# Performance work log

Hardware: AMD Instinct MI355X
Metric: run time of the kernel (lower is better)

Reference implementation:

```python
import jax, jax.numpy as jnp
import numpy as np

EPS_STAB = 1e-9   # numerical_stabilizer default
BN_EPS = 1e-5     # flax BatchNorm default epsilon


def setup_inputs() -> dict:
    key = jax.random.key(0)
    ks = jax.random.split(key, 5)
    B, N, C = 2, 4096, 512
    s = 1.0 / np.sqrt(C)
    d = {"inputs": jax.random.normal(ks[0], (B, N, C), jnp.float32)}
    # 1x1 convs == pointwise linear maps [C_in, C_out] + bias
    for i, w in enumerate(["Wq", "Wk", "Wv", "Wo"]):
        d[w] = jax.random.normal(ks[1 + i], (C, C), jnp.float32) * s
    for b in ["bq", "bk", "bv", "bo"]:
        d[b] = jnp.zeros((C,), jnp.float32)
    # BatchNorm (inference: use_running_average=True since train=False)
    d["bn_scale"] = jnp.ones((C,), jnp.float32)
    d["bn_bias"] = jnp.zeros((C,), jnp.float32)
    d["bn_mean"] = jnp.zeros((C,), jnp.float32)
    d["bn_var"] = jnp.ones((C,), jnp.float32)
    return d


def reference(inputs, Wq, bq, Wk, bk, Wv, bv, Wo, bo,
              bn_scale, bn_bias, bn_mean, bn_var):
    # QKV via 1x1 conv == dense projection. [B, N, C]
    q = inputs @ Wq + bq
    k = inputs @ Wk + bk
    v = inputs @ Wv + bv
    # scores [B, M, N]; softmax over last axis (N)
    att = jax.nn.softmax(jnp.einsum('bmc,bnc->bmn', q, k), axis=-1)
    # non-standard renorm: divide by column sums (axis=1 == M axis)
    att = att / (EPS_STAB + jnp.sum(att, axis=1, keepdims=True))
    # faithful to einsum '...MN,...NC->...NC': sum attention over M, scale v
    out = v * jnp.sum(att, axis=1)[..., None]
    # output 1x1 conv
    out = out @ Wo + bo
    # BatchNorm with running stats (feature axis -1)
    out = (out - bn_mean) * jax.lax.rsqrt(bn_var + BN_EPS) * bn_scale + bn_bias
    return jax.nn.relu(out) + inputs
```

## Files before the change

kernel.cpp:

```cpp
#include <hip/hip_runtime.h>
#include <hip/hip_bf16.h>

typedef unsigned short u16;
typedef unsigned int u32;
typedef __attribute__((ext_vector_type(8))) short short8;
typedef __attribute__((ext_vector_type(4))) float f32x4;
typedef __attribute__((ext_vector_type(4))) unsigned int u32x4;

__device__ __forceinline__ u16 f2bf(float f) {
    union { float f; unsigned u; } v; v.f = f;
    unsigned r = v.u + 0x7fffu + ((v.u >> 16) & 1u);
    return (u16)(r >> 16);
}

__device__ __forceinline__ float fexp2(float x) {
#if __has_builtin(__builtin_amdgcn_exp2f)
    return __builtin_amdgcn_exp2f(x);
#else
    return __expf(x * 0.6931471805599453f);
#endif
}

template <int CTRL>
__device__ __forceinline__ float fdpp(float x) {
    int xi = __builtin_bit_cast(int, x);
    int r = __builtin_amdgcn_update_dpp(0, xi, CTRL, 0xF, 0xF, true);
    return __builtin_bit_cast(float, r);
}
__device__ __forceinline__ float dpp_max16(float m) {
    m = fmaxf(m, fdpp<0xB1>(m));
    m = fmaxf(m, fdpp<0x4E>(m));
    m = fmaxf(m, fdpp<0x141>(m));
    m = fmaxf(m, fdpp<0x140>(m));
    return m;
}
__device__ __forceinline__ float dpp_sum16(float s) {
    s += fdpp<0xB1>(s);
    s += fdpp<0x4E>(s);
    s += fdpp<0x141>(s);
    s += fdpp<0x140>(s);
    return s;
}

#if __has_builtin(__builtin_amdgcn_cvt_pk_fp8_f32) && \
    __has_builtin(__builtin_amdgcn_cvt_f32_fp8)
#define FP8_HW 1
#else
#define FP8_HW 0
#endif

#if !FP8_HW
__device__ __forceinline__ u32 sw_fp8(float x) {
    union { float f; u32 u; } v; v.f = x;
    int E = (int)(v.u >> 23) - 127;
    if (x < 0.001953125f) return 0;
    if (E < -6) return (u32)(x * 512.0f + 0.5f);
    u32 m = v.u & 0x7fffffu;
    u32 r = (m + 0x80000u) >> 20;
    u32 bits = ((u32)(E + 7) << 3) + r;
    return bits > 0x7eu ? 0x7eu : bits;
}
__device__ __forceinline__ float sw_fp8d(u32 b) {
    u32 e = (b >> 3) & 15u, m = b & 7u;
    if (e == 0) return (float)m * 0.001953125f;
    union { u32 u; float f; } v; v.u = ((e + 120u) << 23) | (m << 20);
    return v.f;
}
#endif

__device__ __forceinline__ u32 fp8x4_pack(float p0, float p1, float p2, float p3) {
#if FP8_HW
    u32 v = (u32)__builtin_amdgcn_cvt_pk_fp8_f32(p0, p1, 0, false);
    v = (u32)__builtin_amdgcn_cvt_pk_fp8_f32(p2, p3, (int)v, true);
    return v;
#else
    return sw_fp8(p0) | (sw_fp8(p1) << 8) | (sw_fp8(p2) << 16) | (sw_fp8(p3) << 24);
#endif
}

#if FP8_HW
#define FP8_DEC(v, s) __builtin_amdgcn_cvt_f32_fp8((int)(v), (s))
#else
#define FP8_DEC(v, s) sw_fp8d(((v) >> ((s) * 8)) & 0xffu)
#endif

__device__ __forceinline__ void async_cp16(const u16* g, u16* l) {
    __builtin_amdgcn_global_load_lds(
        (const __attribute__((address_space(1))) void*)g,
        (__attribute__((address_space(3))) void*)l, 16, 0, 0);
}

__device__ __forceinline__ short8 mfma_ld(const u16* base, int off) {
    return *(const short8*)&base[off];
}

__device__ __forceinline__ void gemm512(const u16* __restrict__ A,
                                        const u16* __restrict__ B,
                                        u16* As, u16* Bs,
                                        f32x4 acc[4][4], int tid) {
    const int lane = tid & 63, w = tid >> 6;
    const int quad = lane >> 4, l15 = lane & 15;
    const int wm = tid >> 7, wn = (tid >> 6) & 1;
    const int Gw = lane ^ ((lane >> 3) & 7);
    const int srow = Gw >> 3;
    const int scol = (Gw & 7) * 8;
    const int rl = l15 & 7;
    const int winl = l15 >> 3;
    int Pr[2];
#pragma unroll
    for (int h = 0; h < 2; h++)
        Pr[h] = (rl * 8 + ((quad + h * 4) ^ rl)) * 8;
    const int winA0 = (wm * 64) >> 3, winB0 = (wn * 64) >> 3;
    for (int k0 = 0; k0 < 512; k0 += 64) {
        __syncthreads();
#pragma unroll
        for (int t = 0; t < 4; t++) {
            int win = w * 4 + t;
            async_cp16(A + (size_t)(win * 8 + srow) * 512 + k0 + scol,
                       As + win * 512);
            async_cp16(B + (size_t)(win * 8 + srow) * 512 + k0 + scol,
                       Bs + win * 512);
        }
        __syncthreads();
#pragma unroll
        for (int h = 0; h < 2; h++) {
            short8 af[4], bfr[4];
#pragma unroll
            for (int i = 0; i < 4; i++)
                af[i] = mfma_ld(As, (winA0 + i * 2 + winl) * 512 + Pr[h]);
#pragma unroll
            for (int j = 0; j < 4; j++)
                bfr[j] = mfma_ld(Bs, (winB0 + j * 2 + winl) * 512 + Pr[h]);
#pragma unroll
            for (int i = 0; i < 4; i++)
#pragma unroll
                for (int j = 0; j < 4; j++)
                    acc[i][j] = __builtin_amdgcn_mfma_f32_16x16x32_bf16(
                        af[i], bfr[j], acc[i][j], 0, 0, 0);
        }
    }
}

__device__ __forceinline__ void gemm512_r64(const u16* __restrict__ A,
                                            const u16* __restrict__ B,
                                            u16* As, u16* Bs,
                                            f32x4 acc[2][4], int tid) {
    const int lane = tid & 63, w = tid >> 6;
    const int quad = lane >> 4, l15 = lane & 15;
    const int wm = tid >> 7, wn = (tid >> 6) & 1;
    const int Gw = lane ^ ((lane >> 3) & 7);
    const int srow = Gw >> 3;
    const int scol = (Gw & 7) * 8;
    const int rl = l15 & 7;
    const int winl = l15 >> 3;
    int Pr[2];
#pragma unroll
    for (int h = 0; h < 2; h++)
        Pr[h] = (rl * 8 + ((quad + h * 4) ^ rl)) * 8;
    const int winA0 = (wm * 32) >> 3, winB0 = (wn * 64) >> 3;
    for (int k0 = 0; k0 < 512; k0 += 64) {
        __syncthreads();
#pragma unroll
        for (int t = 0; t < 2; t++) {
            int win = w * 2 + t;
            async_cp16(A + (size_t)(win * 8 + srow) * 512 + k0 + scol,
                       As + win * 512);
        }
#pragma unroll
        for (int t = 0; t < 4; t++) {
            int win = w * 4 + t;
            async_cp16(B + (size_t)(win * 8 + srow) * 512 + k0 + scol,
                       Bs + win * 512);
        }
        __syncthreads();
#pragma unroll
        for (int h = 0; h < 2; h++) {
            short8 af[2], bfr[4];
#pragma unroll
            for (int i = 0; i < 2; i++)
                af[i] = mfma_ld(As, (winA0 + i * 2 + winl) * 512 + Pr[h]);
#pragma unroll
            for (int j = 0; j < 4; j++)
                bfr[j] = mfma_ld(Bs, (winB0 + j * 2 + winl) * 512 + Pr[h]);
#pragma unroll
            for (int i = 0; i < 2; i++)
#pragma unroll
                for (int j = 0; j < 4; j++)
                    acc[i][j] = __builtin_amdgcn_mfma_f32_16x16x32_bf16(
                        af[i], bfr[j], acc[i][j], 0, 0, 0);
        }
    }
}

__global__ void prep(const float* __restrict__ X, const float* __restrict__ W0,
                     const float* __restrict__ W1, const float* __restrict__ W2,
                     const float* __restrict__ W3, u16* __restrict__ Xb,
                     u16* __restrict__ T0, u16* __restrict__ T1,
                     u16* __restrict__ T2, u16* __restrict__ T3,
                     float* __restrict__ Sg) {
    __shared__ float tile[32][33];
    int id = blockIdx.x, tid = threadIdx.x;
    if (id == 5120) {
        float4 z = {0.f, 0.f, 0.f, 0.f};
#pragma unroll
        for (int t = 0; t < 8; t++) ((float4*)Sg)[tid + t * 256] = z;
        return;
    }
    if (id < 4096) {
        int idx = (id * 256 + tid) * 4;
        float4 v = *(const float4*)&X[idx];
        ushort4 o;
        o.x = f2bf(v.x); o.y = f2bf(v.y); o.z = f2bf(v.z); o.w = f2bf(v.w);
        *(ushort4*)&Xb[idx] = o;
        return;
    }
    int t = id - 4096;
    int z = t >> 8, rem = t & 255;
    int bo_ = (rem & 15) * 32, bi = (rem >> 4) * 32;
    const float* src; u16* dst;
    switch (z) {
        case 0: src = W0; dst = T0; break;
        case 1: src = W1; dst = T1; break;
        case 2: src = W2; dst = T2; break;
        default: src = W3; dst = T3; break;
    }
    int tx = tid & 31, ty = tid >> 5;
#pragma unroll
    for (int s = 0; s < 4; s++) {
        int i = bi + ty + s * 8;
        tile[ty + s * 8][tx] = src[i * 512 + bo_ + tx];
    }
    __syncthreads();
#pragma unroll
    for (int s = 0; s < 4; s++) {
        int o = bo_ + ty + s * 8;
        dst[o * 512 + bi + tx] = f2bf(tile[tx][ty + s * 8]);
    }
}

__global__ __launch_bounds__(256) void gemm_qkv(
    const u16* __restrict__ Xb, const u16* __restrict__ Wall,
    const float* __restrict__ bq, const float* __restrict__ bk,
    const float* __restrict__ bv, u16* __restrict__ Qall) {
    __shared__ __align__(16) u16 As[8192];
    __shared__ __align__(16) u16 Bs[8192];
    int tid = threadIdx.x;
    int m0 = blockIdx.x * 128, n0 = blockIdx.y * 128, z = blockIdx.z;
    const u16* Bt = Wall + (size_t)z * 262144 + (size_t)n0 * 512;
    const float* bias = (z == 0) ? bq : (z == 1) ? bk : bv;
    const float qs = (z == 0) ? 1.44269504088896340736f : 1.0f;
    u16* C = Qall + (size_t)z * 4194304;
    f32x4 acc[4][4];
#pragma unroll
    for (int i = 0; i < 4; i++)
#pragma unroll
        for (int j = 0; j < 4; j++) acc[i][j] = (f32x4){0.f, 0.f, 0.f, 0.f};
    gemm512(Xb + (size_t)m0 * 512, Bt, As, Bs, acc, tid);
    int lane = tid & 63, quad = lane >> 4, l15 = lane & 15;
    int wm = tid >> 7, wn = (tid >> 6) & 1;
#pragma unroll
    for (int j = 0; j < 4; j++) {
        int n = n0 + wn * 64 + j * 16 + l15;
        float bvv = bias[n];
#pragma unroll
        for (int i = 0; i < 4; i++)
#pragma unroll
            for (int rg = 0; rg < 4; rg++) {
                int m = m0 + wm * 64 + i * 16 + quad * 4 + rg;
                C[(size_t)m * 512 + n] = f2bf((acc[i][j][rg] + bvv) * qs);
            }
    }
}

__device__ __forceinline__ void stage_half_A(const u16* __restrict__ Q,
                                             u16* dst, int kn, int half,
                                             int wid, int srow, int scol) {
#pragma unroll
    for (int c = 0; c < 2; c++) {
        int win = (wid >> 2) * 16 + half * 8 + (wid & 3) * 2 + c;
        async_cp16(Q + (size_t)(win * 8 + srow) * 512 + kn + scol,
                   dst + win * 512);
    }
}
__device__ __forceinline__ void stage_half_B(const u16* __restrict__ K,
                                             u16* dst, int kn, int half,
                                             int wid, int srow, int scol) {
#pragma unroll
    for (int c = 0; c < 2; c++) {
        int win = (wid >> 1) * 8 + half * 4 + (wid & 1) * 2 + c;
        async_cp16(K + (size_t)(win * 8 + srow) * 512 + kn + scol,
                   dst + win * 512);
    }
}

__global__ __launch_bounds__(512, 2) void attn_pass1p(
    const u16* __restrict__ Qb, const u16* __restrict__ Kb,
    float2* __restrict__ statsP, u32* __restrict__ Pbuf) {
    __shared__ __align__(16) u16 As[2][16384];
    __shared__ __align__(16) u16 Bs[2][16384];
    int tid = threadIdx.x;
    int mblk = blockIdx.x, nblk = blockIdx.y, b = blockIdx.z;
    const u16* Q = Qb + ((size_t)(b * 4096 + mblk * 256)) * 512;
    const u16* K = Kb + ((size_t)(b * 4096 + nblk * 256)) * 512;
    int lane = tid & 63, wid = tid >> 6;
    int quad = lane >> 4, l15 = lane & 15;
    int wm = wid >> 2, wn = wid & 3;
    int Gw = lane ^ ((lane >> 3) & 7);
    int srow = Gw >> 3, scol = (Gw & 7) * 8;
    int rl = l15 & 7, winl = l15 >> 3;
    int Pr[2];
#pragma unroll
    for (int h = 0; h < 2; h++)
        Pr[h] = (rl * 8 + ((quad + h * 4) ^ rl)) * 8;

    f32x4 acc[8][4];
#pragma unroll
    for (int i = 0; i < 8; i++)
#pragma unroll
        for (int j = 0; j < 4; j++) acc[i][j] = (f32x4){0.f, 0.f, 0.f, 0.f};

    stage_half_A(Q, &As[0][0], 0, 0, wid, srow, scol);
    stage_half_B(K, &Bs[0][0], 0, 0, wid, srow, scol);
    stage_half_B(K, &Bs[0][0], 0, 1, wid, srow, scol);
    stage_half_A(Q, &As[0][0], 0, 1, wid, srow, scol);
    asm volatile("s_waitcnt vmcnt(0)" ::: "memory");
    __builtin_amdgcn_s_barrier();
    asm volatile("" ::: "memory");

    for (int kt = 0; kt < 8; ++kt) {
        const u16* Ac = &As[kt & 1][0];
        const u16* Bc = &Bs[kt & 1][0];
        u16* An = &As[(kt + 1) & 1][0];
        u16* Bn = &Bs[(kt + 1) & 1][0];
        int kn = (kt + 1) * 64;
        bool pf = (kt < 7);
        short8 af[4][2], bf0[2][2], bf1[2][2];
#pragma unroll
        for (int ph = 0; ph < 4; ++ph) {
            const int ih = ph >> 1;
            const int jh = (ph ^ (ph >> 1)) & 1;
            if (ph == 0) {
#pragma unroll
                for (int h = 0; h < 2; h++)
#pragma unroll
                    for (int ii = 0; ii < 4; ii++)
                        af[ii][h] = mfma_ld(
                            Ac, (wm * 16 + ii * 2 + winl) * 512 + Pr[h]);
#pragma unroll
                for (int h = 0; h < 2; h++)
#pragma unroll
                    for (int jj = 0; jj < 2; jj++)
                        bf0[jj][h] = mfma_ld(
                            Bc, (wn * 8 + jj * 2 + winl) * 512 + Pr[h]);
            } else if (ph == 1) {
#pragma unroll
                for (int h = 0; h < 2; h++)
#pragma unroll
                    for (int jj = 0; jj < 2; jj++)
                        bf1[jj][h] = mfma_ld(
                            Bc, (wn * 8 + 4 + jj * 2 + winl) * 512 + Pr[h]);
            } else if (ph == 2) {
#pragma unroll
                for (int h = 0; h < 2; h++)
#pragma unroll
                    for (int ii = 0; ii < 4; ii++)
                        af[ii][h] = mfma_ld(
                            Ac, (wm * 16 + 8 + ii * 2 + winl) * 512 + Pr[h]);
            }
            if (pf) {
                if (ph == 0) {
                    stage_half_A(Q, An, kn, 0, wid, srow, scol);
                    stage_half_B(K, Bn, kn, 0, wid, srow, scol);
                } else if (ph == 1) {
                    stage_half_B(K, Bn, kn, 1, wid, srow, scol);
                } else if (ph == 2) {
                    stage_half_A(Q, An, kn, 1, wid, srow, scol);
                }
            }
            if (ph == 1) {
                if (pf) asm volatile("s_waitcnt vmcnt(6)" ::: "memory");
                else    asm volatile("s_waitcnt vmcnt(0)" ::: "memory");
            }
            if (ph == 3) asm volatile("s_waitcnt vmcnt(2)" ::: "memory");
            asm volatile("" ::: "memory");
            __builtin_amdgcn_s_barrier();
            asm volatile("s_waitcnt lgkmcnt(0)" ::: "memory");
            __builtin_amdgcn_s_setprio(1);
            if (jh == 0) {
#pragma unroll
                for (int h = 0; h < 2; h++)
#pragma unroll
                    for (int ii = 0; ii < 4; ii++)
#pragma unroll
                        for (int jj = 0; jj < 2; jj++)
                            acc[ih * 4 + ii][jj] =
                                __builtin_amdgcn_mfma_f32_16x16x32_bf16(
                                    af[ii][h], bf0[jj][h],
                                    acc[ih * 4 + ii][jj], 0, 0, 0);
            } else {
#pragma unroll
                for (int h = 0; h < 2; h++)
#pragma unroll
                    for (int ii = 0; ii < 4; ii++)
#pragma unroll
                        for (int jj = 0; jj < 2; jj++)
                            acc[ih * 4 + ii][2 + jj] =
                                __builtin_amdgcn_mfma_f32_16x16x32_bf16(
                                    af[ii][h], bf1[jj][h],
                                    acc[ih * 4 + ii][2 + jj], 0, 0, 0);
            }
            __builtin_amdgcn_s_setprio(0);
            asm volatile("" ::: "memory");
            __builtin_amdgcn_s_barrier();
            asm volatile("" ::: "memory");
        }
    }

    u32* Pt = Pbuf + ((size_t)((b * 16 + mblk) * 16 + nblk)) * 16384;
    int ch = nblk * 4 + wn;
    float2* Sp = statsP + ((size_t)(b * 64 + ch)) * 4096;
    int mbase = mblk * 256 + wm * 128;
#pragma unroll
    for (int i = 0; i < 8; i++) {
        u32x4 pk;
#pragma unroll
        for (int rg = 0; rg < 4; rg++) {
            float v0 = acc[i][0][rg], v1 = acc[i][1][rg];
            float v2 = acc[i][2][rg], v3 = acc[i][3][rg];
            float Mt = fmaxf(fmaxf(v0, v1), fmaxf(v2, v3));
            Mt = dpp_max16(Mt);
            float e8 = Mt - 8.0f;
            float p0 = fexp2(v0 - e8), p1 = fexp2(v1 - e8);
            float p2 = fexp2(v2 - e8), p3 = fexp2(v3 - e8);
            pk[rg] = fp8x4_pack(p0, p1, p2, p3);
            float L = dpp_sum16(p0 + p1 + p2 + p3);
            if (l15 == 0)
                Sp[mbase + i * 16 + quad * 4 + rg] =
                    make_float2(Mt, L * 0.00390625f);
        }
        *(u32x4*)&Pt[i * 2048 + tid * 4] = pk;
    }
}

__global__ void reduce_stats2(const float2* __restrict__ statsP,
                              float* __restrict__ cstat) {
    int t = blockIdx.x * 256 + threadIdx.x;
    int b = t >> 12, m = t & 4095;
    const float2* sp = statsP + (size_t)b * 64 * 4096 + m;
    float M = -INFINITY;
#pragma unroll 4
    for (int ch = 0; ch < 64; ch++) M = fmaxf(M, sp[(size_t)ch * 4096].x);
    float Z = 0.f;
#pragma unroll 4
    for (int ch = 0; ch < 64; ch++) {
        float2 p = sp[(size_t)ch * 4096];
        Z += p.y * fexp2(p.x - M);
    }
    cstat[t] = M + __log2f(Z);
}

__global__ __launch_bounds__(512) void colsum(
    const u32* __restrict__ Pbuf, const float2* __restrict__ statsP,
    const float* __restrict__ cstat, float* __restrict__ Sg) {
    int tid = threadIdx.x, lane = tid & 63, wid = tid >> 6;
    int quad = lane >> 4, l15 = lane & 15;
    int wm = wid >> 2, wn = wid & 3;
    int nblk = blockIdx.x, mgrp = blockIdx.y, b = blockIdx.z;
    int ch = nblk * 4 + wn;
    const float2* Sp = statsP + ((size_t)(b * 64 + ch)) * 4096;
    const float* Cp = cstat + (size_t)b * 4096;
    float cp[4] = {0.f, 0.f, 0.f, 0.f};
    for (int mb = 0; mb < 2; mb++) {
        int mblk = mgrp * 2 + mb;
        const u32* Pt =
            Pbuf + ((size_t)((b * 16 + mblk) * 16 + nblk)) * 16384;
#pragma unroll
        for (int i = 0; i < 8; i++) {
            int r0 = mblk * 256 + wm * 128 + i * 16 + quad * 4;
            float4 s01 = *(const float4*)&Sp[r0];
            float4 s23 = *(const float4*)&Sp[r0 + 2];
            float4 cv = *(const float4*)&Cp[r0];
            float fv[4] = {fexp2(s01.x - 8.0f - cv.x),
                           fexp2(s01.z - 8.0f - cv.y),
                           fexp2(s23.x - 8.0f - cv.z),
                           fexp2(s23.z - 8.0f - cv.w)};
            float fm = fmaxf(fmaxf(fv[0], fv[1]), fmaxf(fv[2], fv[3]));
            if (fm > 3.469446951953614e-18f) {
                u32x4 e4 = *(const u32x4*)&Pt[i * 2048 + tid * 4];
#pragma unroll
                for (int rg = 0; rg < 4; rg++) {
                    u32 e = e4[rg];
                    cp[0] += FP8_DEC(e, 0) * fv[rg];
                    cp[1] += FP8_DEC(e, 1) * fv[rg];
                    cp[2] += FP8_DEC(e, 2) * fv[rg];
                    cp[3] += FP8_DEC(e, 3) * fv[rg];
                }
            }
        }
    }
#pragma unroll
    for (int j = 0; j < 4; j++) {
        float s = cp[j];
        s += __shfl_xor(s, 16);
        s += __shfl_xor(s, 32);
        if (lane < 16)
            atomicAdd(&Sg[b * 4096 + nblk * 256 + wn * 64 + j * 16 + l15], s);
    }
}

__global__ __launch_bounds__(256) void gemm_final(
    const u16* __restrict__ A, const u16* __restrict__ Bt,
    const float* __restrict__ Sg, const float* __restrict__ bo,
    const float* __restrict__ g, const float* __restrict__ bb,
    const float* __restrict__ mean, const float* __restrict__ var,
    const float* __restrict__ X, float* __restrict__ out) {
    __shared__ __align__(16) u16 As[4096];
    __shared__ __align__(16) u16 Bs[8192];
    int tid = threadIdx.x;
    int m0 = blockIdx.x * 64, n0 = blockIdx.y * 128;
    f32x4 acc[2][4];
#pragma unroll
    for (int i = 0; i < 2; i++)
#pragma unroll
        for (int j = 0; j < 4; j++) acc[i][j] = (f32x4){0.f, 0.f, 0.f, 0.f};
    gemm512_r64(A + (size_t)m0 * 512, Bt + (size_t)n0 * 512, As, Bs, acc, tid);
    int lane = tid & 63, quad = lane >> 4, l15 = lane & 15;
    int wm = tid >> 7, wn = (tid >> 6) & 1;
    float sc[2][4];
#pragma unroll
    for (int i = 0; i < 2; i++) {
        float4 s = *(const float4*)&Sg[m0 + wm * 32 + i * 16 + quad * 4];
        float v[4] = {s.x, s.y, s.z, s.w};
#pragma unroll
        for (int rg = 0; rg < 4; rg++) sc[i][rg] = v[rg] / (1e-9f + v[rg]);
    }
#pragma unroll
    for (int j = 0; j < 4; j++) {
        int n = n0 + wn * 64 + j * 16 + l15;
        float aj = rsqrtf(var[n] + 1e-5f) * g[n];
        float cj = bb[n] - mean[n] * aj;
        float bj = bo[n];
#pragma unroll
        for (int i = 0; i < 2; i++)
#pragma unroll
            for (int rg = 0; rg < 4; rg++) {
                int m = m0 + wm * 32 + i * 16 + quad * 4 + rg;
                float x = acc[i][j][rg] * sc[i][rg] + bj;
                float y = x * aj + cj;
                out[(size_t)m * 512 + n] = fmaxf(y, 0.f) + X[(size_t)m * 512 + n];
            }
    }
}

extern "C" void kernel_launch(void* const* d_in, const int* in_sizes, int n_in,
                              void* d_out, int out_size, void* d_ws, size_t ws_size,
                              hipStream_t stream) {
    const float* X  = (const float*)d_in[0];
    const float* Wq = (const float*)d_in[1];
    const float* Wk = (const float*)d_in[2];
    const float* Wv = (const float*)d_in[3];
    const float* Wo = (const float*)d_in[4];
    const float* bq = (const float*)d_in[5];
    const float* bk = (const float*)d_in[6];
    const float* bv = (const float*)d_in[7];
    const float* bo = (const float*)d_in[8];
    const float* g    = (const float*)d_in[9];
    const float* bb   = (const float*)d_in[10];
    const float* mean = (const float*)d_in[11];
    const float* var  = (const float*)d_in[12];
    float* out = (float*)d_out;

    char* ws = (char*)d_ws;
    u16* Xb  = (u16*)(ws + 0);
    u16* Wqt = (u16*)(ws + 8388608);
    u16* Wot = (u16*)(ws + 9961472);
    u16* Qb  = (u16*)(ws + 10485760);
    u16* Kb  = (u16*)(ws + 18874368);
    u16* Vb  = (u16*)(ws + 27262976);
    float2* statsP = (float2*)(ws + 35651584);
    float* Sg      = (float*)(ws + 39845888);
    float* cstat   = (float*)(ws + 39878656);
    u32* Pbuf      = (u32*)(ws + 39911424);

    prep<<<5121, 256, 0, stream>>>(X, Wq, Wk, Wv, Wo, Xb, Wqt, Wqt + 262144,
                                   Wqt + 524288, Wot, Sg);
    gemm_qkv<<<dim3(64, 4, 3), 256, 0, stream>>>(Xb, Wqt, bq, bk, bv, Qb);
    attn_pass1p<<<dim3(16, 16, 2), 512, 0, stream>>>(Qb, Kb, statsP, Pbuf);
    reduce_stats2<<<32, 256, 0, stream>>>(statsP, cstat);
    colsum<<<dim3(16, 8, 2), 512, 0, stream>>>(Pbuf, statsP, cstat, Sg);
    gemm_final<<<dim3(128, 4), 256, 0, stream>>>(Vb, Wot, Sg, bo, g, bb, mean, var,
                                                 X, out);
}
```

Baseline: 203.9 us.

## Reuse pipelined 256x256 attention GEMM core for QKV projection

```diff
diff --git a/kernel.cpp b/kernel.cpp
--- a/kernel.cpp
+++ b/kernel.cpp
@@ -94,49 +94,137 @@
     return *(const short8*)&base[off];
 }
 
-__device__ __forceinline__ void gemm512(const u16* __restrict__ A,
+__device__ __forceinline__ void stage_half_A(const u16* __restrict__ Q,
+                                             u16* dst, int kn, int half,
+                                             int wid, int srow, int scol) {
+#pragma unroll
+    for (int c = 0; c < 2; c++) {
+        int win = (wid >> 2) * 16 + half * 8 + (wid & 3) * 2 + c;
+        async_cp16(Q + (size_t)(win * 8 + srow) * 512 + kn + scol,
+                   dst + win * 512);
+    }
+}
+__device__ __forceinline__ void stage_half_B(const u16* __restrict__ K,
+                                             u16* dst, int kn, int half,
+                                             int wid, int srow, int scol) {
+#pragma unroll
+    for (int c = 0; c < 2; c++) {
+        int win = (wid >> 1) * 8 + half * 4 + (wid & 1) * 2 + c;
+        async_cp16(K + (size_t)(win * 8 + srow) * 512 + kn + scol,
+                   dst + win * 512);
+    }
+}
+
+__device__ __forceinline__ void core256(const u16* __restrict__ A,
                                         const u16* __restrict__ B,
-                                        u16* As, u16* Bs,
-                                        f32x4 acc[4][4], int tid) {
-    const int lane = tid & 63, w = tid >> 6;
-    const int quad = lane >> 4, l15 = lane & 15;
-    const int wm = tid >> 7, wn = (tid >> 6) & 1;
-    const int Gw = lane ^ ((lane >> 3) & 7);
-    const int srow = Gw >> 3;
-    const int scol = (Gw & 7) * 8;
-    const int rl = l15 & 7;
-    const int winl = l15 >> 3;
+                                        u16* As0, u16* As1,
+                                        u16* Bs0, u16* Bs1,
+                                        f32x4 acc[8][4], int tid) {
+    int lane = tid & 63, wid = tid >> 6;
+    int quad = lane >> 4, l15 = lane & 15;
+    int wm = wid >> 2, wn = wid & 3;
+    int Gw = lane ^ ((lane >> 3) & 7);
+    int srow = Gw >> 3, scol = (Gw & 7) * 8;
+    int rl = l15 & 7, winl = l15 >> 3;
     int Pr[2];
 #pragma unroll
     for (int h = 0; h < 2; h++)
         Pr[h] = (rl * 8 + ((quad + h * 4) ^ rl)) * 8;
-    const int winA0 = (wm * 64) >> 3, winB0 = (wn * 64) >> 3;
-    for (int k0 = 0; k0 < 512; k0 += 64) {
-        __syncthreads();
-#pragma unroll
-        for (int t = 0; t < 4; t++) {
-            int win = w * 4 + t;
-            async_cp16(A + (size_t)(win * 8 + srow) * 512 + k0 + scol,
-                       As + win * 512);
-            async_cp16(B + (size_t)(win * 8 + srow) * 512 + k0 + scol,
-                       Bs + win * 512);
-        }
-        __syncthreads();
-#pragma unroll
-        for (int h = 0; h < 2; h++) {
-            short8 af[4], bfr[4];
-#pragma unroll
-            for (int i = 0; i < 4; i++)
-                af[i] = mfma_ld(As, (winA0 + i * 2 + winl) * 512 + Pr[h]);
-#pragma unroll
-            for (int j = 0; j < 4; j++)
-                bfr[j] = mfma_ld(Bs, (winB0 + j * 2 + winl) * 512 + Pr[h]);
-#pragma unroll
-            for (int i = 0; i < 4; i++)
-#pragma unroll
-                for (int j = 0; j < 4; j++)
-                    acc[i][j] = __builtin_amdgcn_mfma_f32_16x16x32_bf16(
-                        af[i], bfr[j], acc[i][j], 0, 0, 0);
+
+    stage_half_A(A, As0, 0, 0, wid, srow, scol);
+    stage_half_B(B, Bs0, 0, 0, wid, srow, scol);
+    stage_half_B(B, Bs0, 0, 1, wid, srow, scol);
+    stage_half_A(A, As0, 0, 1, wid, srow, scol);
+    asm volatile("s_waitcnt vmcnt(0)" ::: "memory");
+    __builtin_amdgcn_s_barrier();
+    asm volatile("" ::: "memory");
+
+    for (int kt = 0; kt < 8; ++kt) {
+        const u16* Ac = (kt & 1) ? As1 : As0;
+        const u16* Bc = (kt & 1) ? Bs1 : Bs0;
+        u16* An = (kt & 1) ? As0 : As1;
+        u16* Bn = (kt & 1) ? Bs0 : Bs1;
+        int kn = (kt + 1) * 64;
+        bool pf = (kt < 7);
+        short8 af[4][2], bf0[2][2], bf1[2][2];
+#pragma unroll
+        for (int ph = 0; ph < 4; ++ph) {
+            const int ih = ph >> 1;
+            const int jh = (ph ^ (ph >> 1)) & 1;
+            if (ph == 0) {
+#pragma unroll
+                for (int h = 0; h < 2; h++)
+#pragma unroll
+                    for (int ii = 0; ii < 4; ii++)
+                        af[ii][h] = mfma_ld(
+                            Ac, (wm * 16 + ii * 2 + winl) * 512 + Pr[h]);
+#pragma unroll
+                for (int h = 0; h < 2; h++)
+#pragma unroll
+                    for (int jj = 0; jj < 2; jj++)
+                        bf0[jj][h] = mfma_ld(
+                            Bc, (wn * 8 + jj * 2 + winl) * 512 + Pr[h]);
+            } else if (ph == 1) {
+#pragma unroll
+                for (int h = 0; h < 2; h++)
+#pragma unroll
+                    for (int jj = 0; jj < 2; jj++)
+                        bf1[jj][h] = mfma_ld(
+                            Bc, (wn * 8 + 4 + jj * 2 + winl) * 512 + Pr[h]);
+            } else if (ph == 2) {
+#pragma unroll
+                for (int h = 0; h < 2; h++)
+#pragma unroll
+                    for (int ii = 0; ii < 4; ii++)
+                        af[ii][h] = mfma_ld(
+                            Ac, (wm * 16 + 8 + ii * 2 + winl) * 512 + Pr[h]);
+            }
+            if (pf) {
+                if (ph == 0) {
+                    stage_half_A(A, An, kn, 0, wid, srow, scol);
+                    stage_half_B(B, Bn, kn, 0, wid, srow, scol);
+                } else if (ph == 1) {
+                    stage_half_B(B, Bn, kn, 1, wid, srow, scol);
+                } else if (ph == 2) {
+                    stage_half_A(A, An, kn, 1, wid, srow, scol);
+                }
+            }
+            if (ph == 1) {
+                if (pf) asm volatile("s_waitcnt vmcnt(6)" ::: "memory");
+                else    asm volatile("s_waitcnt vmcnt(0)" ::: "memory");
+            }
+            if (ph == 3) asm volatile("s_waitcnt vmcnt(2)" ::: "memory");
+            asm volatile("" ::: "memory");
+            __builtin_amdgcn_s_barrier();
+            asm volatile("s_waitcnt lgkmcnt(0)" ::: "memory");
+            __builtin_amdgcn_s_setprio(1);
+            if (jh == 0) {
+#pragma unroll
+                for (int h = 0; h < 2; h++)
+#pragma unroll
+                    for (int ii = 0; ii < 4; ii++)
+#pragma unroll
+                        for (int jj = 0; jj < 2; jj++)
+                            acc[ih * 4 + ii][jj] =
+                                __builtin_amdgcn_mfma_f32_16x16x32_bf16(
+                                    af[ii][h], bf0[jj][h],
+                                    acc[ih * 4 + ii][jj], 0, 0, 0);
+            } else {
+#pragma unroll
+                for (int h = 0; h < 2; h++)
+#pragma unroll
+                    for (int ii = 0; ii < 4; ii++)
+#pragma unroll
+                        for (int jj = 0; jj < 2; jj++)
+                            acc[ih * 4 + ii][2 + jj] =
+                                __builtin_amdgcn_mfma_f32_16x16x32_bf16(
+                                    af[ii][h], bf1[jj][h],
+                                    acc[ih * 4 + ii][2 + jj], 0, 0, 0);
+            }
+            __builtin_amdgcn_s_setprio(0);
+            asm volatile("" ::: "memory");
+            __builtin_amdgcn_s_barrier();
+            asm volatile("" ::: "memory");
         }
     }
 }
@@ -238,58 +326,40 @@
     }
 }
 
-__global__ __launch_bounds__(256) void gemm_qkv(
+__global__ __launch_bounds__(512, 2) void gemm_qkv(
     const u16* __restrict__ Xb, const u16* __restrict__ Wall,
     const float* __restrict__ bq, const float* __restrict__ bk,
     const float* __restrict__ bv, u16* __restrict__ Qall) {
-    __shared__ __align__(16) u16 As[8192];
-    __shared__ __align__(16) u16 Bs[8192];
+    __shared__ __align__(16) u16 As[2][16384];
+    __shared__ __align__(16) u16 Bs[2][16384];
     int tid = threadIdx.x;
-    int m0 = blockIdx.x * 128, n0 = blockIdx.y * 128, z = blockIdx.z;
-    const u16* Bt = Wall + (size_t)z * 262144 + (size_t)n0 * 512;
+    int m0 = blockIdx.x * 256, n0 = blockIdx.y * 256, z = blockIdx.z;
+    const u16* A = Xb + (size_t)m0 * 512;
+    const u16* B = Wall + (size_t)z * 262144 + (size_t)n0 * 512;
+    f32x4 acc[8][4];
+#pragma unroll
+    for (int i = 0; i < 8; i++)
+#pragma unroll
+        for (int j = 0; j < 4; j++) acc[i][j] = (f32x4){0.f, 0.f, 0.f, 0.f};
+    core256(A, B, &As[0][0], &As[1][0], &Bs[0][0], &Bs[1][0], acc, tid);
+
     const float* bias = (z == 0) ? bq : (z == 1) ? bk : bv;
     const float qs = (z == 0) ? 1.44269504088896340736f : 1.0f;
     u16* C = Qall + (size_t)z * 4194304;
-    f32x4 acc[4][4];
-#pragma unroll
-    for (int i = 0; i < 4; i++)
-#pragma unroll
-        for (int j = 0; j < 4; j++) acc[i][j] = (f32x4){0.f, 0.f, 0.f, 0.f};
-    gemm512(Xb + (size_t)m0 * 512, Bt, As, Bs, acc, tid);
-    int lane = tid & 63, quad = lane >> 4, l15 = lane & 15;
-    int wm = tid >> 7, wn = (tid >> 6) & 1;
+    int lane = tid & 63, wid = tid >> 6;
+    int quad = lane >> 4, l15 = lane & 15;
+    int wm = wid >> 2, wn = wid & 3;
 #pragma unroll
     for (int j = 0; j < 4; j++) {
         int n = n0 + wn * 64 + j * 16 + l15;
         float bvv = bias[n];
 #pragma unroll
-        for (int i = 0; i < 4; i++)
+        for (int i = 0; i < 8; i++)
 #pragma unroll
             for (int rg = 0; rg < 4; rg++) {
-                int m = m0 + wm * 64 + i * 16 + quad * 4 + rg;
+                int m = m0 + wm * 128 + i * 16 + quad * 4 + rg;
                 C[(size_t)m * 512 + n] = f2bf((acc[i][j][rg] + bvv) * qs);
             }
-    }
-}
-
-__device__ __forceinline__ void stage_half_A(const u16* __restrict__ Q,
-                                             u16* dst, int kn, int half,
-                                             int wid, int srow, int scol) {
-#pragma unroll
-    for (int c = 0; c < 2; c++) {
-        int win = (wid >> 2) * 16 + half * 8 + (wid & 3) * 2 + c;
-        async_cp16(Q + (size_t)(win * 8 + srow) * 512 + kn + scol,
-                   dst + win * 512);
-    }
-}
-__device__ __forceinline__ void stage_half_B(const u16* __restrict__ K,
-                                             u16* dst, int kn, int half,
-                                             int wid, int srow, int scol) {
-#pragma unroll
-    for (int c = 0; c < 2; c++) {
-        int win = (wid >> 1) * 8 + half * 4 + (wid & 1) * 2 + c;
-        async_cp16(K + (size_t)(win * 8 + srow) * 512 + kn + scol,
-                   dst + win * 512);
     }
 }
 
@@ -305,116 +375,13 @@
     int lane = tid & 63, wid = tid >> 6;
     int quad = lane >> 4, l15 = lane & 15;
     int wm = wid >> 2, wn = wid & 3;
-    int Gw = lane ^ ((lane >> 3) & 7);
-    int srow = Gw >> 3, scol = (Gw & 7) * 8;
-    int rl = l15 & 7, winl = l15 >> 3;
-    int Pr[2];
-#pragma unroll
-    for (int h = 0; h < 2; h++)
-        Pr[h] = (rl * 8 + ((quad + h * 4) ^ rl)) * 8;
 
     f32x4 acc[8][4];
 #pragma unroll
     for (int i = 0; i < 8; i++)
 #pragma unroll
         for (int j = 0; j < 4; j++) acc[i][j] = (f32x4){0.f, 0.f, 0.f, 0.f};
-
-    stage_half_A(Q, &As[0][0], 0, 0, wid, srow, scol);
-    stage_half_B(K, &Bs[0][0], 0, 0, wid, srow, scol);
-    stage_half_B(K, &Bs[0][0], 0, 1, wid, srow, scol);
-    stage_half_A(Q, &As[0][0], 0, 1, wid, srow, scol);
-    asm volatile("s_waitcnt vmcnt(0)" ::: "memory");
-    __builtin_amdgcn_s_barrier();
-    asm volatile("" ::: "memory");
-
-    for (int kt = 0; kt < 8; ++kt) {
-        const u16* Ac = &As[kt & 1][0];
-        const u16* Bc = &Bs[kt & 1][0];
-        u16* An = &As[(kt + 1) & 1][0];
-        u16* Bn = &Bs[(kt + 1) & 1][0];
-        int kn = (kt + 1) * 64;
-        bool pf = (kt < 7);
-        short8 af[4][2], bf0[2][2], bf1[2][2];
-#pragma unroll
-        for (int ph = 0; ph < 4; ++ph) {
-            const int ih = ph >> 1;
-            const int jh = (ph ^ (ph >> 1)) & 1;
-            if (ph == 0) {
-#pragma unroll
-                for (int h = 0; h < 2; h++)
-#pragma unroll
-                    for (int ii = 0; ii < 4; ii++)
-                        af[ii][h] = mfma_ld(
-                            Ac, (wm * 16 + ii * 2 + winl) * 512 + Pr[h]);
-#pragma unroll
-                for (int h = 0; h < 2; h++)
-#pragma unroll
-                    for (int jj = 0; jj < 2; jj++)
-                        bf0[jj][h] = mfma_ld(
-                            Bc, (wn * 8 + jj * 2 + winl) * 512 + Pr[h]);
-            } else if (ph == 1) {
-#pragma unroll
-                for (int h = 0; h < 2; h++)
-#pragma unroll
-                    for (int jj = 0; jj < 2; jj++)
-                        bf1[jj][h] = mfma_ld(
-                            Bc, (wn * 8 + 4 + jj * 2 + winl) * 512 + Pr[h]);
-            } else if (ph == 2) {
-#pragma unroll
-                for (int h = 0; h < 2; h++)
-#pragma unroll
-                    for (int ii = 0; ii < 4; ii++)
-                        af[ii][h] = mfma_ld(
-                            Ac, (wm * 16 + 8 + ii * 2 + winl) * 512 + Pr[h]);
-            }
-            if (pf) {
-                if (ph == 0) {
-                    stage_half_A(Q, An, kn, 0, wid, srow, scol);
-                    stage_half_B(K, Bn, kn, 0, wid, srow, scol);
-                } else if (ph == 1) {
-                    stage_half_B(K, Bn, kn, 1, wid, srow, scol);
-                } else if (ph == 2) {
-                    stage_half_A(Q, An, kn, 1, wid, srow, scol);
-                }
-            }
-            if (ph == 1) {
-                if (pf) asm volatile("s_waitcnt vmcnt(6)" ::: "memory");
-                else    asm volatile("s_waitcnt vmcnt(0)" ::: "memory");
-            }
-            if (ph == 3) asm volatile("s_waitcnt vmcnt(2)" ::: "memory");
-            asm volatile("" ::: "memory");
-            __builtin_amdgcn_s_barrier();
-            asm volatile("s_waitcnt lgkmcnt(0)" ::: "memory");
-            __builtin_amdgcn_s_setprio(1);
-            if (jh == 0) {
-#pragma unroll
-                for (int h = 0; h < 2; h++)
-#pragma unroll
-                    for (int ii = 0; ii < 4; ii++)
-#pragma unroll
-                        for (int jj = 0; jj < 2; jj++)
-                            acc[ih * 4 + ii][jj] =
-                                __builtin_amdgcn_mfma_f32_16x16x32_bf16(
-                                    af[ii][h], bf0[jj][h],
-                                    acc[ih * 4 + ii][jj], 0, 0, 0);
-            } else {
-#pragma unroll
-                for (int h = 0; h < 2; h++)
-#pragma unroll
-                    for (int ii = 0; ii < 4; ii++)
-#pragma unroll
-                        for (int jj = 0; jj < 2; jj++)
-                            acc[ih * 4 + ii][2 + jj] =
-                                __builtin_amdgcn_mfma_f32_16x16x32_bf16(
-                                    af[ii][h], bf1[jj][h],
-                                    acc[ih * 4 + ii][2 + jj], 0, 0, 0);
-            }
-            __builtin_amdgcn_s_setprio(0);
-            asm volatile("" ::: "memory");
-            __builtin_amdgcn_s_barrier();
-            asm volatile("" ::: "memory");
-        }
-    }
+    core256(Q, K, &As[0][0], &As[1][0], &Bs[0][0], &Bs[1][0], acc, tid);
 
     u32* Pt = Pbuf + ((size_t)((b * 16 + mblk) * 16 + nblk)) * 16384;
     int ch = nblk * 4 + wn;
@@ -584,7 +551,7 @@
 
     prep<<<5121, 256, 0, stream>>>(X, Wq, Wk, Wv, Wo, Xb, Wqt, Wqt + 262144,
                                    Wqt + 524288, Wot, Sg);
-    gemm_qkv<<<dim3(64, 4, 3), 256, 0, stream>>>(Xb, Wqt, bq, bk, bv, Qb);
+    gemm_qkv<<<dim3(32, 2, 3), 512, 0, stream>>>(Xb, Wqt, bq, bk, bv, Qb);
     attn_pass1p<<<dim3(16, 16, 2), 512, 0, stream>>>(Qb, Kb, statsP, Pbuf);
     reduce_stats2<<<32, 256, 0, stream>>>(statsP, cstat);
     colsum<<<dim3(16, 8, 2), 512, 0, stream>>>(Pbuf, statsP, cstat, Sg);
```

Measured after the change: 200.6 us, median of 2. About the same (-1.6%).
